# Optimization experiments

Measured on AMD Instinct MI355X. Metric: run time of the kernel, lower is better.

## Reference

```python
import jax, jax.numpy as jnp
import numpy as np

T = 0.1          # temperature from module
NORM_EPS = 1e-12 # F.normalize default eps
COS_EPS = 1e-6   # nn.CosineSimilarity eps

def setup_inputs() -> dict:
    key = jax.random.key(0)
    k1, k2, k3 = jax.random.split(key, 3)
    B, D = 8192, 2048
    return {
        "embed": jax.random.normal(k1, (B, D), dtype=jnp.float32),
        "embed_enhance": jax.random.normal(k2, (B, D), dtype=jnp.float32),
        "labels": jax.random.uniform(k3, (B,), dtype=jnp.float32),
    }

def reference(embed, embed_enhance, labels):
    # Faithful to the original module, INCLUDING the early `return loss`
    # inside the `for i` loop: only i == 0 contributes.
    labels = labels.astype(jnp.float32)
    B = embed.shape[0]
    # F.normalize(embed, dim=-1)
    en = embed / jnp.maximum(jnp.linalg.norm(embed, axis=-1, keepdims=True), NORM_EPS)
    a = en[0]                                                # [D], normalized anchor
    na = jnp.maximum(jnp.linalg.norm(a), COS_EPS)
    nb = jnp.maximum(jnp.linalg.norm(embed_enhance, axis=-1), COS_EPS)  # [B]
    cos = (embed_enhance @ a) / (na * nb)                    # [B] cosine sims vs row 0
    mask = jnp.arange(B) != 0                                # exclude j == i == 0
    neg = -cos / T                                           # = log(exp(-cos/t))
    E0 = 1e-12 + jnp.sum(jnp.where(mask, jnp.exp(neg), 0.0))
    C0 = 1e-12 + jnp.sum(jnp.where(mask, labels[0] * labels, 0.0))
    Cij = labels[0] * labels / C0                            # [B]
    L0 = jnp.sum(jnp.where(mask, -Cij * (neg - jnp.log(E0)), 0.0))
    return L0 / B
```

## Files before the change

kernel.cpp:

```cpp
#include <hip/hip_runtime.h>
#include <math.h>

static constexpr int Dn = 2048;
static constexpr int Bn = 8192;
static constexpr int NBLK  = 1024;
static constexpr int NWAVE = NBLK * 4;

__device__ __forceinline__ float dot4(float4 a, float4 b) {
    return a.x * b.x + a.y * b.y + a.z * b.z + a.w * b.w;
}

__global__ __launch_bounds__(256) void k_main(const float* __restrict__ embed,
                                              const float* __restrict__ ee,
                                              const float* __restrict__ labels,
                                              double* __restrict__ part) {
    const int t    = threadIdx.x;
    const int lane = t & 63;
    const int wv   = ((int)blockIdx.x << 2) | (t >> 6);

    const float4* e0 = reinterpret_cast<const float4*>(embed);
    float4 av[8];
    float ss = 0.f;
#pragma unroll
    for (int s = 0; s < 8; ++s) {
        av[s] = e0[(s << 6) + lane];
        ss += dot4(av[s], av[s]);
    }
#pragma unroll
    for (int o = 32; o > 0; o >>= 1) ss += __shfl_xor(ss, o, 64);
    const float inv = 1.0f / fmaxf(sqrtf(ss), 1e-12f);

    float ssa = 0.f;
#pragma unroll
    for (int s = 0; s < 8; ++s) {
        av[s].x *= inv; av[s].y *= inv; av[s].z *= inv; av[s].w *= inv;
        ssa += dot4(av[s], av[s]);
    }
#pragma unroll
    for (int o = 32; o > 0; o >>= 1) ssa += __shfl_xor(ssa, o, 64);
    const float na = fmaxf(sqrtf(ssa), 1e-6f);

    double sE = 0.0, sL = 0.0, sN = 0.0;
    for (int j = wv; j < Bn; j += NWAVE) {
        const float4* row = reinterpret_cast<const float4*>(ee + (size_t)j * Dn);
        float dt = 0.f, sr = 0.f;
#pragma unroll
        for (int s = 0; s < 8; ++s) {
            const float4 r = row[(s << 6) + lane];
            dt += dot4(r, av[s]);
            sr += dot4(r, r);
        }
#pragma unroll
        for (int o = 32; o > 0; o >>= 1) {
            dt += __shfl_xor(dt, o, 64);
            sr += __shfl_xor(sr, o, 64);
        }
        if (lane == 0 && j != 0) {
            const float nb  = fmaxf(sqrtf(sr), 1e-6f);
            const float neg = -10.0f * dt / (na * nb);
            const double lb = (double)labels[j];
            sE += (double)expf(neg);
            sL += lb;
            sN += lb * (double)neg;
        }
    }
    if (lane == 0) {
        part[wv]             = sE;
        part[NWAVE + wv]     = sL;
        part[2 * NWAVE + wv] = sN;
    }
}

__global__ __launch_bounds__(256) void k_final(const double* __restrict__ part,
                                               const float* __restrict__ labels,
                                               float* __restrict__ out) {
    __shared__ double rE[4], rL[4], rN[4];
    const int t = threadIdx.x;
    const int lane = t & 63, wave = t >> 6;

    double sE = 0.0, sL = 0.0, sN = 0.0;
    for (int i = t; i < NWAVE; i += 256) {
        sE += part[i];
        sL += part[NWAVE + i];
        sN += part[2 * NWAVE + i];
    }
#pragma unroll
    for (int o = 32; o > 0; o >>= 1) {
        sE += __shfl_down(sE, o, 64);
        sL += __shfl_down(sL, o, 64);
        sN += __shfl_down(sN, o, 64);
    }
    if (lane == 0) { rE[wave] = sE; rL[wave] = sL; rN[wave] = sN; }
    __syncthreads();
    if (t == 0) {
        const double E0 = 1e-12 + rE[0] + rE[1] + rE[2] + rE[3];
        const double S2 = rL[0] + rL[1] + rL[2] + rL[3];
        const double S3 = rN[0] + rN[1] + rN[2] + rN[3];
        const double l0 = (double)labels[0];
        const double C0 = 1e-12 + l0 * S2;
        const double L0 = -(l0 / C0) * (S3 - log(E0) * S2);
        out[0] = (float)(L0 / (double)Bn);
    }
}

extern "C" void kernel_launch(void* const* d_in, const int* in_sizes, int n_in,
                              void* d_out, int out_size, void* d_ws, size_t ws_size,
                              hipStream_t stream) {
    const float* embed  = (const float*)d_in[0];
    const float* ee     = (const float*)d_in[1];
    const float* labels = (const float*)d_in[2];
    float* out = (float*)d_out;

    double* part = (double*)d_ws;

    k_main<<<NBLK, 256, 0, stream>>>(embed, ee, labels, part);
    k_final<<<1, 256, 0, stream>>>(part, labels, out);
}
```

Measured before the change: 128.4 us.

## Halve grid, double-buffer row loads with nontemporal prefetch and preload labels

Halves the block count so each wave handles four rows, and fully unrolls the row loop. The next row is prefetched into registers while the current one is reduced, using nontemporal loads for the streamed embed_enhance data. Labels are loaded up front. This aims to overlap memory latency with compute and cut per-block overhead, at the cost of more registers and fewer waves in flight to hide latency.

New measurement: 132.6 us. +3.3%, slower.

```diff
diff --git a/kernel.cpp b/kernel.cpp
--- a/kernel.cpp
+++ b/kernel.cpp
@@ -3,10 +3,13 @@
 
 static constexpr int Dn = 2048;
 static constexpr int Bn = 8192;
-static constexpr int NBLK  = 1024;
+static constexpr int NBLK  = 512;
 static constexpr int NWAVE = NBLK * 4;
+static constexpr int ROWS  = Bn / NWAVE;
 
-__device__ __forceinline__ float dot4(float4 a, float4 b) {
+typedef float f4 __attribute__((ext_vector_type(4)));
+
+__device__ __forceinline__ float dot4(f4 a, f4 b) {
     return a.x * b.x + a.y * b.y + a.z * b.z + a.w * b.w;
 }
 
@@ -18,8 +21,8 @@
     const int lane = t & 63;
     const int wv   = ((int)blockIdx.x << 2) | (t >> 6);
 
-    const float4* e0 = reinterpret_cast<const float4*>(embed);
-    float4 av[8];
+    const f4* e0 = reinterpret_cast<const f4*>(embed);
+    f4 av[8];
     float ss = 0.f;
 #pragma unroll
     for (int s = 0; s < 8; ++s) {
@@ -33,22 +36,41 @@
     float ssa = 0.f;
 #pragma unroll
     for (int s = 0; s < 8; ++s) {
-        av[s].x *= inv; av[s].y *= inv; av[s].z *= inv; av[s].w *= inv;
+        av[s] *= inv;
         ssa += dot4(av[s], av[s]);
     }
 #pragma unroll
     for (int o = 32; o > 0; o >>= 1) ssa += __shfl_xor(ssa, o, 64);
     const float na = fmaxf(sqrtf(ssa), 1e-6f);
 
+    float lb[ROWS];
+    if (lane == 0) {
+#pragma unroll
+        for (int r = 0; r < ROWS; ++r) lb[r] = labels[wv + r * NWAVE];
+    }
+
     double sE = 0.0, sL = 0.0, sN = 0.0;
-    for (int j = wv; j < Bn; j += NWAVE) {
-        const float4* row = reinterpret_cast<const float4*>(ee + (size_t)j * Dn);
+    f4 cur[8], nxt[8];
+    {
+        const f4* row = reinterpret_cast<const f4*>(ee + (size_t)wv * Dn);
+#pragma unroll
+        for (int s = 0; s < 8; ++s)
+            cur[s] = __builtin_nontemporal_load(&row[(s << 6) + lane]);
+    }
+#pragma unroll
+    for (int r = 0; r < ROWS; ++r) {
+        const int j = wv + r * NWAVE;
+        if (r + 1 < ROWS) {
+            const f4* rn = reinterpret_cast<const f4*>(ee + (size_t)(j + NWAVE) * Dn);
+#pragma unroll
+            for (int s = 0; s < 8; ++s)
+                nxt[s] = __builtin_nontemporal_load(&rn[(s << 6) + lane]);
+        }
         float dt = 0.f, sr = 0.f;
 #pragma unroll
         for (int s = 0; s < 8; ++s) {
-            const float4 r = row[(s << 6) + lane];
-            dt += dot4(r, av[s]);
-            sr += dot4(r, r);
+            dt += dot4(cur[s], av[s]);
+            sr += dot4(cur[s], cur[s]);
         }
 #pragma unroll
         for (int o = 32; o > 0; o >>= 1) {
@@ -58,11 +80,12 @@
         if (lane == 0 && j != 0) {
             const float nb  = fmaxf(sqrtf(sr), 1e-6f);
             const float neg = -10.0f * dt / (na * nb);
-            const double lb = (double)labels[j];
             sE += (double)expf(neg);
-            sL += lb;
-            sN += lb * (double)neg;
+            sL += (double)lb[r];
+            sN += (double)lb[r] * (double)neg;
         }
+#pragma unroll
+        for (int s = 0; s < 8; ++s) cur[s] = nxt[s];
     }
     if (lane == 0) {
         part[wv]             = sE;
```
